# Performance work log

Hardware: AMD Instinct MI355X
Metric: run time of the kernel (lower is better)

The kernel has to match this reference:

```python
import jax, jax.numpy as jnp
import numpy as np

BORDER = 8
NMS_THRESH = 0.0
NMS_KSIZE = 5
TOP_K = 512
GAUSS_KSIZE = 15
GAUSS_SIGMA = 0.5
LOSS_LAMBDA = 1.0


def filter_border(x, border=BORDER):
    B, C, H, W = x.shape
    mask = jnp.zeros((H, W), x.dtype).at[border:H - border, border:W - border].set(1.0)
    return x * mask


def _bilinear_sample(img, x, y):
    # img: [H,W]; x,y: [H,W] float pixel coords in src frame; zeros outside.
    H, W = img.shape
    x0 = jnp.floor(x)
    y0 = jnp.floor(y)
    wx1 = x - x0
    wy1 = y - y0

    def gather(yy, xx):
        valid = (xx >= 0) & (xx <= W - 1) & (yy >= 0) & (yy <= H - 1)
        xi = jnp.clip(xx, 0, W - 1).astype(jnp.int32)
        yi = jnp.clip(yy, 0, H - 1).astype(jnp.int32)
        return img[yi, xi] * valid.astype(img.dtype)

    return ((1 - wy1) * (1 - wx1) * gather(y0, x0)
            + (1 - wy1) * wx1 * gather(y0, x0 + 1)
            + wy1 * (1 - wx1) * gather(y0 + 1, x0)
            + wy1 * wx1 * gather(y0 + 1, x0 + 1))


def warp_image(ref, src, homo):
    # Sample src at homo-mapped coords of ref's pixel grid -> output in ref frame.
    B, _, H, W = ref.shape
    ys, xs = jnp.meshgrid(jnp.arange(H, dtype=ref.dtype), jnp.arange(W, dtype=ref.dtype), indexing='ij')
    pts = jnp.stack([xs.ravel(), ys.ravel(), jnp.ones(H * W, ref.dtype)], 0)  # [3, HW]
    mapped = jnp.einsum('bij,jn->bin', homo, pts)  # [B,3,HW]
    x = (mapped[:, 0] / mapped[:, 2]).reshape(B, H, W)
    y = (mapped[:, 1] / mapped[:, 2]).reshape(B, H, W)
    out = jax.vmap(_bilinear_sample)(src[:, 0], x, y)  # [B,H,W]
    return out[:, None]


def select_keypoints(score, thresh, ksize, top_k):
    B, _, H, W = score.shape
    pooled = jax.lax.reduce_window(score, -jnp.inf, jax.lax.max,
                                   (1, 1, ksize, ksize), (1, 1, 1, 1), 'SAME')
    keep = (score == pooled) & (score > thresh)
    s = jnp.where(keep, score, 0.0)
    flat = s.reshape(B, H * W)
    vals, idx = jax.lax.top_k(flat, top_k)
    out = jnp.zeros_like(flat).at[jnp.arange(B)[:, None], idx].set(vals)
    kp = jnp.stack([idx // W, idx % W], -1)  # [B, top_k, 2] (y, x)
    return out.reshape(B, 1, H, W), kp


def gaussian_filter(x, ksize, sigma):
    ax = jnp.arange(ksize, dtype=x.dtype) - (ksize - 1) / 2.0
    g = jnp.exp(-(ax ** 2) / (2.0 * sigma ** 2))
    g = g / g.sum()
    k2 = jnp.outer(g, g)[None, None]  # [1,1,k,k]
    return jax.lax.conv_general_dilated(x, k2, (1, 1), 'SAME')


def setup_inputs() -> dict:
    key = jax.random.key(0)
    k1, k2, k3 = jax.random.split(key, 3)
    B, H, W = 16, 480, 640
    score1 = jax.random.uniform(k1, (B, 1, H, W), jnp.float32)
    score2 = jax.random.uniform(k2, (B, 1, H, W), jnp.float32)
    # Near-identity pixel-space homographies: small rotation/shear/perspective + a few px translation.
    scale = jnp.array([[0.01, 0.01, 2.0],
                       [0.01, 0.01, 2.0],
                       [1e-5, 1e-5, 0.0]], jnp.float32)
    homo12 = jnp.eye(3, dtype=jnp.float32) + jax.random.normal(k3, (B, 3, 3), jnp.float32) * scale
    return {"score1": score1, "score2": score2, "homo12": homo12}


def reference(score1, score2, homo12):
    score2 = filter_border(score2)
    w_score2 = warp_image(score1, score2, homo12)
    vis_mask = jnp.ones_like(score2)
    vis_mask1 = (warp_image(score1, vis_mask, homo12) > 0).astype(score1.dtype)
    s1, kp1 = select_keypoints(score1, NMS_THRESH, NMS_KSIZE, TOP_K)
    s1 = gaussian_filter(s1, GAUSS_KSIZE, GAUSS_SIGMA)
    gt_s1, _ = select_keypoints(w_score2, NMS_THRESH, NMS_KSIZE, TOP_K)
    gt_s1 = gaussian_filter(gt_s1, GAUSS_KSIZE, GAUSS_SIGMA)
    norm = vis_mask1.sum()
    loss = (((s1 - gt_s1) ** 2) * vis_mask1 / norm).sum() * LOSS_LAMBDA
    return (loss, kp1, vis_mask1)
```

## Files before the change

### kernel.cpp

```cpp
#include <hip/hip_runtime.h>
#include <cstdint>
#include <cstddef>

#define BN 16
#define HH 480
#define WW 640
#define HWSZ (HH*WW)
#define CAP 32768
#define TOPK 512
#define RED_BLOCKS 2048
#define NTX 64
#define NTY 32

typedef unsigned long long u64;

#define W2_OFF   0ULL
#define W2_SZ    ((unsigned long long)BN*HWSZ*4ULL)
#define MAPS_OFF (W2_OFF + W2_SZ)
#define MAPS_SZ  (2ULL*BN*HWSZ*4ULL)
#define CAND_OFF (MAPS_OFF + MAPS_SZ)
#define CAND_SZ  (2ULL*BN*CAP*8ULL)
#define CNT_OFF  (CAND_OFF + CAND_SZ)
#define CNT_SZ   (4096ULL)
#define SEL_OFF  (CNT_OFF + CNT_SZ)
#define SEL_SZ   (2ULL*BN*TOPK*8ULL)
#define PART_OFF (SEL_OFF + SEL_SZ)
#define PART_SZ  ((unsigned long long)RED_BLOCKS*2*4ULL)

__global__ void k_warp_vis(const float* __restrict__ score2,
                           const float* __restrict__ homo,
                           float* __restrict__ w2,
                           float* __restrict__ vis,
                           unsigned int* __restrict__ cnt,
                           float* __restrict__ maps) {
    if (blockIdx.x == 0) {
        for (int i = threadIdx.x; i < 1024; i += 256) cnt[i] = 0u;
    }
    int t = blockIdx.x * 256 + threadIdx.x;
    {
        float4 z4 = make_float4(0.f, 0.f, 0.f, 0.f);
        *reinterpret_cast<float4*>(maps + (size_t)t * 8)     = z4;
        *reinterpret_cast<float4*>(maps + (size_t)t * 8 + 4) = z4;
    }
    int b = t / (HWSZ / 4);
    int q = t - b * (HWSZ / 4);
    int p = q * 4;
    int py = p / WW, px = p - py * WW;
    const float* h = homo + b * 9;
    const float* sb = score2 + (size_t)b * HWSZ;

    float4 wout;
    float vout[4];
    #pragma unroll
    for (int u = 0; u < 4; ++u) {
        float fx = (float)(px + u), fy = (float)py;
        float X = h[0] * fx + h[1] * fy + h[2];
        float Y = h[3] * fx + h[4] * fy + h[5];
        float Z = h[6] * fx + h[7] * fy + h[8];
        float x = X / Z, y = Y / Z;
        float x0 = floorf(x), y0 = floorf(y);
        float wx = x - x0, wy = y - y0;
        float vv[4], gv[4];
        #pragma unroll
        for (int j = 0; j < 2; ++j) {
            #pragma unroll
            for (int i = 0; i < 2; ++i) {
                float xx = x0 + (float)i;
                float yy = y0 + (float)j;
                bool valid = (xx >= 0.f) && (xx <= (float)(WW - 1)) &&
                             (yy >= 0.f) && (yy <= (float)(HH - 1));
                int xi = (int)fminf(fmaxf(xx, 0.f), (float)(WW - 1));
                int yi = (int)fminf(fmaxf(yy, 0.f), (float)(HH - 1));
                float v = sb[yi * WW + xi];
                bool inb = (xi >= 8) && (xi < WW - 8) && (yi >= 8) && (yi < HH - 8);
                vv[j * 2 + i] = (valid && inb) ? v : 0.f;
                gv[j * 2 + i] = valid ? 1.f : 0.f;
            }
        }
        float w00 = (1.f - wy) * (1.f - wx), w01 = (1.f - wy) * wx;
        float w10 = wy * (1.f - wx),         w11 = wy * wx;
        float val = w00 * vv[0] + w01 * vv[1] + w10 * vv[2] + w11 * vv[3];
        float vsm = w00 * gv[0] + w01 * gv[1] + w10 * gv[2] + w11 * gv[3];
        ((float*)&wout)[u] = val;
        vout[u] = (vsm > 0.f) ? 1.f : 0.f;
    }
    int base = b * HWSZ + p;
    *reinterpret_cast<float4*>(w2 + base) = wout;
    vis[base + 0] = vout[0];
    vis[base + 1] = vout[1];
    vis[base + 2] = vout[2];
    vis[base + 3] = vout[3];
}

__global__ void k_nms(const float* __restrict__ s1,
                      const float* __restrict__ w2,
                      u64* __restrict__ cand,
                      unsigned int* __restrict__ cnt) {
    __shared__ float tile[NTY + 4][NTX + 4];
    __shared__ float colmax[NTY][NTX + 4];
    __shared__ unsigned int s_loc, s_base;
    int z = blockIdx.z;
    const float* sb = (z < BN) ? (s1 + (size_t)z * HWSZ)
                               : (w2 + (size_t)(z - BN) * HWSZ);
    int tid = threadIdx.x;
    int bx0 = blockIdx.x * NTX, by0 = blockIdx.y * NTY;
    if (tid == 0) s_loc = 0;

    for (int i = tid; i < (NTY + 4) * (NTX + 4); i += 256) {
        int ly = i / (NTX + 4), lx = i - ly * (NTX + 4);
        int gy = by0 + ly - 2, gx = bx0 + lx - 2;
        float v = -__builtin_inff();
        if ((unsigned)gy < (unsigned)HH && (unsigned)gx < (unsigned)WW)
            v = sb[gy * WW + gx];
        tile[ly][lx] = v;
    }
    __syncthreads();

    for (int i = tid; i < NTY * (NTX + 4); i += 256) {
        int y = i / (NTX + 4), x = i - y * (NTX + 4);
        float m = tile[y][x];
        m = fmaxf(m, tile[y + 1][x]);
        m = fmaxf(m, tile[y + 2][x]);
        m = fmaxf(m, tile[y + 3][x]);
        m = fmaxf(m, tile[y + 4][x]);
        colmax[y][x] = m;
    }
    __syncthreads();

    int ox = tid & 63, oyb = (tid >> 6) * 8;
    bool fl[8];
    float vv[8];
    unsigned int pos[8];
    #pragma unroll
    for (int k = 0; k < 8; ++k) {
        int oy = oyb + k;
        float v = tile[oy + 2][ox + 2];
        float m = colmax[oy][ox];
        m = fmaxf(m, colmax[oy][ox + 1]);
        m = fmaxf(m, colmax[oy][ox + 2]);
        m = fmaxf(m, colmax[oy][ox + 3]);
        m = fmaxf(m, colmax[oy][ox + 4]);
        fl[k] = (v == m) && (v > 0.f);
        vv[k] = v;
        if (fl[k]) pos[k] = atomicAdd(&s_loc, 1u);
    }
    __syncthreads();
    if (tid == 0 && s_loc) s_base = atomicAdd(&cnt[z * 32], s_loc);
    __syncthreads();
    #pragma unroll
    for (int k = 0; k < 8; ++k) {
        if (fl[k]) {
            unsigned int off = s_base + pos[k];
            if (off < CAP) {
                int p = (by0 + oyb + k) * WW + bx0 + ox;
                cand[(size_t)z * CAP + off] =
                    ((u64)__float_as_uint(vv[k]) << 32) | (u64)(~(unsigned)p);
            }
        }
    }
}

__global__ __launch_bounds__(1024) void k_topk(const u64* __restrict__ cand,
                                               const unsigned int* __restrict__ cnt,
                                               u64* __restrict__ sel,
                                               float* __restrict__ kp_out) {
    int s = blockIdx.x;
    int tid = threadIdx.x;
    int n = (int)cnt[s * 32];
    if (n > CAP) n = CAP;
    const u64* keys = cand + (size_t)s * CAP;

    __shared__ unsigned int histw[16][256];
    __shared__ unsigned int hist[256];
    __shared__ u64 skeys[TOPK];
    __shared__ int s_digit, s_krem, s_done;
    __shared__ unsigned int s_cnt;

    int wid = tid >> 6;

    if (n > TOPK) {
        u64 prefix = 0ULL;
        int krem = TOPK;
        for (int lvl = 7; lvl >= 0; --lvl) {
            for (int i = tid; i < 16 * 256; i += 1024) ((unsigned int*)histw)[i] = 0u;
            if (tid == 0) s_done = 0;
            __syncthreads();
            int shift = lvl * 8;
            u64 pmask = (lvl == 7) ? 0ULL : (~0ULL << (shift + 8));
            for (int i = tid; i < n; i += 1024) {
                u64 k = keys[i];
                if ((k & pmask) == prefix)
                    atomicAdd(&histw[wid][(unsigned int)((k >> shift) & 0xFF)], 1u);
            }
            __syncthreads();
            if (tid < 256) {
                unsigned int sum = 0;
                #pragma unroll
                for (int w = 0; w < 16; ++w) sum += histw[w][tid];
                hist[tid] = sum;
            }
            __syncthreads();
            for (int off = 1; off < 256; off <<= 1) {
                unsigned int add = 0;
                if (tid < 256 - off) add = hist[tid + off];
                __syncthreads();
                if (tid < 256) hist[tid] += add;
                __syncthreads();
            }
            if (tid < 256) {
                unsigned int ge = hist[tid];
                unsigned int gt = (tid < 255) ? hist[tid + 1] : 0u;
                if (ge >= (unsigned)krem && gt < (unsigned)krem) {
                    s_digit = tid; s_krem = krem - (int)gt;
                    if (ge == (unsigned)krem) s_done = 1;
                }
            }
            __syncthreads();
            prefix |= ((u64)s_digit) << shift;
            krem = s_krem;
            int done = s_done;
            __syncthreads();
            if (done) break;
        }
        if (tid == 0) s_cnt = 0;
        __syncthreads();
        for (int i = tid; i < n; i += 1024) {
            u64 k = keys[i];
            if (k >= prefix) {
                unsigned int pos = atomicAdd(&s_cnt, 1u);
                if (pos < TOPK) skeys[pos] = k;
            }
        }
        __syncthreads();
        for (int i = (int)s_cnt + tid; i < TOPK; i += 1024) skeys[i] = 0ULL;
    } else {
        for (int i = tid; i < TOPK; i += 1024) skeys[i] = (i < n) ? keys[i] : 0ULL;
    }
    __syncthreads();

    if (s < BN) {
        for (int k = 2; k <= TOPK; k <<= 1) {
            for (int j = k >> 1; j > 0; j >>= 1) {
                if (tid < 256) {
                    int i = (tid % j) + (tid / j) * (j << 1);
                    int l = i + j;
                    bool desc = ((i & k) == 0);
                    u64 a = skeys[i], c = skeys[l];
                    if ((a < c) == desc) { skeys[i] = c; skeys[l] = a; }
                }
                __syncthreads();
            }
        }
    }

    for (int i = tid; i < TOPK; i += 1024) {
        u64 k = skeys[i];
        sel[(size_t)s * TOPK + i] = k;
        if (s < BN) {
            unsigned int idx = ~(unsigned int)(k & 0xFFFFFFFFULL);
            int y = (int)(idx / WW), x = (int)(idx - (unsigned int)y * WW);
            kp_out[(size_t)(s * TOPK + i) * 2 + 0] = (float)y;
            kp_out[(size_t)(s * TOPK + i) * 2 + 1] = (float)x;
        }
    }
}

__global__ void k_stamp(const u64* __restrict__ sel,
                        float* __restrict__ maps) {
    int idx = blockIdx.x * 256 + threadIdx.x;
    int gi = idx / 225;
    int t  = idx - gi * 225;
    u64 k = sel[gi];
    float val = __uint_as_float((unsigned int)(k >> 32));
    if (val <= 0.f) return;
    unsigned int pidx = ~(unsigned int)(k & 0xFFFFFFFFULL);
    int py = (int)(pidx / WW), px = (int)(pidx - (unsigned int)py * WW);
    int dy = t / 15 - 7, dx = t - (dy + 7) * 15 - 7;
    int yy = py + dy, xx = px + dx;
    if (yy < 0 || yy >= HH || xx < 0 || xx >= WW) return;
    const float inv_s2 = 0.61869347f;
    float ga = __expf(-2.f * (float)(dy * dy));
    float gb = __expf(-2.f * (float)(dx * dx));
    int m = gi >> 13, b = (gi >> 9) & 15;
    atomicAdd(&maps[((size_t)m * BN + b) * HWSZ + yy * WW + xx], val * ga * gb * inv_s2);
}

__global__ void k_reduce(const float* __restrict__ maps,
                         const float* __restrict__ vis,
                         float* __restrict__ partial) {
    const int N = BN * HWSZ;
    float lp = 0.f, vsum = 0.f;
    int stride = RED_BLOCKS * 256 * 4;
    for (int i = (blockIdx.x * 256 + threadIdx.x) * 4; i < N; i += stride) {
        float4 m0 = *reinterpret_cast<const float4*>(maps + i);
        float4 m1 = *reinterpret_cast<const float4*>(maps + N + i);
        float v0 = vis[i + 0], v1 = vis[i + 1], v2 = vis[i + 2], v3 = vis[i + 3];
        float d0 = m0.x - m1.x, d1 = m0.y - m1.y, d2 = m0.z - m1.z, d3 = m0.w - m1.w;
        lp += d0 * d0 * v0 + d1 * d1 * v1 + d2 * d2 * v2 + d3 * d3 * v3;
        vsum += v0 + v1 + v2 + v3;
    }
    #pragma unroll
    for (int off = 32; off > 0; off >>= 1) {
        lp   += __shfl_down(lp, off);
        vsum += __shfl_down(vsum, off);
    }
    __shared__ float sl[4], sv[4];
    int w = threadIdx.x >> 6, ln = threadIdx.x & 63;
    if (ln == 0) { sl[w] = lp; sv[w] = vsum; }
    __syncthreads();
    if (threadIdx.x == 0) {
        partial[blockIdx.x * 2 + 0] = sl[0] + sl[1] + sl[2] + sl[3];
        partial[blockIdx.x * 2 + 1] = sv[0] + sv[1] + sv[2] + sv[3];
    }
}

__global__ void k_final(const float* __restrict__ partial, float* __restrict__ out) {
    float a = 0.f, c = 0.f;
    for (int i = threadIdx.x; i < RED_BLOCKS; i += 256) {
        a += partial[i * 2 + 0];
        c += partial[i * 2 + 1];
    }
    #pragma unroll
    for (int off = 32; off > 0; off >>= 1) {
        a += __shfl_down(a, off);
        c += __shfl_down(c, off);
    }
    __shared__ float sl[4], sv[4];
    int w = threadIdx.x >> 6, ln = threadIdx.x & 63;
    if (ln == 0) { sl[w] = a; sv[w] = c; }
    __syncthreads();
    if (threadIdx.x == 0)
        out[0] = (sl[0] + sl[1] + sl[2] + sl[3]) / (sv[0] + sv[1] + sv[2] + sv[3]);
}

extern "C" void kernel_launch(void* const* d_in, const int* in_sizes, int n_in,
                              void* d_out, int out_size, void* d_ws, size_t ws_size,
                              hipStream_t stream) {
    const float* score1 = (const float*)d_in[0];
    const float* score2 = (const float*)d_in[1];
    const float* homo   = (const float*)d_in[2];
    float* out = (float*)d_out;
    char* ws = (char*)d_ws;

    float* w2          = (float*)(ws + W2_OFF);
    float* maps        = (float*)(ws + MAPS_OFF);
    u64* cand          = (u64*)(ws + CAND_OFF);
    unsigned int* cnt  = (unsigned int*)(ws + CNT_OFF);
    u64* sel           = (u64*)(ws + SEL_OFF);
    float* partial     = (float*)(ws + PART_OFF);

    float* kp_out  = out + 1;
    float* vis_out = out + 1 + (size_t)BN * TOPK * 2;

    k_warp_vis<<<BN * HWSZ / (256 * 4), 256, 0, stream>>>(score2, homo, w2, vis_out, cnt, maps);

    dim3 g(WW / NTX, HH / NTY, 2 * BN);
    k_nms<<<g, 256, 0, stream>>>(score1, w2, cand, cnt);

    k_topk<<<32, 1024, 0, stream>>>(cand, cnt, sel, kp_out);

    k_stamp<<<(2 * BN * TOPK * 225) / 256, 256, 0, stream>>>(sel, maps);

    k_reduce<<<RED_BLOCKS, 256, 0, stream>>>(maps, vis_out, partial);
    k_final<<<1, 256, 0, stream>>>(partial, out);
}
```

Measured before the change: 202.7 us.

## Compact top-k candidates into shared memory, ballot NMS offsets, fuse final reduction

Top-k radix select now copies the surviving candidates into a shared-memory buffer once the selected bucket is small enough, so later histogram passes read shared memory instead of rescanning global memory. The scan over 256 bins uses a single-wave shuffle scan in place of a barrier-heavy shared-memory loop. NMS uses wave ballots and popcounts instead of per-element shared atomics. The final loss reduction is folded into the last k_reduce block via an atomic counter, which removes one launch but relies on that counter being zeroed each call.

```diff
diff --git a/kernel.cpp b/kernel.cpp
--- a/kernel.cpp
+++ b/kernel.cpp
@@ -11,6 +11,7 @@
 #define RED_BLOCKS 2048
 #define NTX 64
 #define NTY 32
+#define CBUF 1536
 
 typedef unsigned long long u64;
 
@@ -98,13 +99,13 @@
                       unsigned int* __restrict__ cnt) {
     __shared__ float tile[NTY + 4][NTX + 4];
     __shared__ float colmax[NTY][NTX + 4];
-    __shared__ unsigned int s_loc, s_base;
+    __shared__ unsigned int wcnt[4];
+    __shared__ unsigned int s_base;
     int z = blockIdx.z;
     const float* sb = (z < BN) ? (s1 + (size_t)z * HWSZ)
                                : (w2 + (size_t)(z - BN) * HWSZ);
     int tid = threadIdx.x;
     int bx0 = blockIdx.x * NTX, by0 = blockIdx.y * NTY;
-    if (tid == 0) s_loc = 0;
 
     for (int i = tid; i < (NTY + 4) * (NTX + 4); i += 256) {
         int ly = i / (NTX + 4), lx = i - ly * (NTX + 4);
@@ -128,9 +129,12 @@
     __syncthreads();
 
     int ox = tid & 63, oyb = (tid >> 6) * 8;
+    int wid = tid >> 6, lane = tid & 63;
+    u64 lt_mask = (1ULL << lane) - 1ULL;
     bool fl[8];
     float vv[8];
-    unsigned int pos[8];
+    unsigned int off_k[8];
+    unsigned int wtot = 0;
     #pragma unroll
     for (int k = 0; k < 8; ++k) {
         int oy = oyb + k;
@@ -142,15 +146,24 @@
         m = fmaxf(m, colmax[oy][ox + 4]);
         fl[k] = (v == m) && (v > 0.f);
         vv[k] = v;
-        if (fl[k]) pos[k] = atomicAdd(&s_loc, 1u);
-    }
-    __syncthreads();
-    if (tid == 0 && s_loc) s_base = atomicAdd(&cnt[z * 32], s_loc);
+        u64 bal = __ballot(fl[k]);
+        off_k[k] = wtot + (unsigned)__popcll(bal & lt_mask);
+        wtot += (unsigned)__popcll(bal);
+    }
+    if (lane == 0) wcnt[wid] = wtot;
+    __syncthreads();
+    if (tid == 0) {
+        unsigned tot = wcnt[0] + wcnt[1] + wcnt[2] + wcnt[3];
+        unsigned base = tot ? atomicAdd(&cnt[z * 32], tot) : 0u;
+        unsigned acc = base;
+        #pragma unroll
+        for (int w = 0; w < 4; ++w) { unsigned c = wcnt[w]; wcnt[w] = acc; acc += c; }
+    }
     __syncthreads();
     #pragma unroll
     for (int k = 0; k < 8; ++k) {
         if (fl[k]) {
-            unsigned int off = s_base + pos[k];
+            unsigned off = wcnt[wid] + off_k[k];
             if (off < CAP) {
                 int p = (by0 + oyb + k) * WW + bx0 + ox;
                 cand[(size_t)z * CAP + off] =
@@ -168,27 +181,31 @@
     int tid = threadIdx.x;
     int n = (int)cnt[s * 32];
     if (n > CAP) n = CAP;
-    const u64* keys = cand + (size_t)s * CAP;
+    const u64* gkeys = cand + (size_t)s * CAP;
 
     __shared__ unsigned int histw[16][256];
     __shared__ unsigned int hist[256];
     __shared__ u64 skeys[TOPK];
-    __shared__ int s_digit, s_krem, s_done;
+    __shared__ u64 cbuf[CBUF];
+    __shared__ int s_digit, s_krem, s_done, s_ge, s_nc;
     __shared__ unsigned int s_cnt;
 
-    int wid = tid >> 6;
+    int wid = tid >> 6, lane = tid & 63;
 
     if (n > TOPK) {
         u64 prefix = 0ULL;
         int krem = TOPK;
+        bool comp = false;
+        int nsrc = n;
         for (int lvl = 7; lvl >= 0; --lvl) {
             for (int i = tid; i < 16 * 256; i += 1024) ((unsigned int*)histw)[i] = 0u;
             if (tid == 0) s_done = 0;
             __syncthreads();
+            const u64* src = comp ? cbuf : gkeys;
             int shift = lvl * 8;
             u64 pmask = (lvl == 7) ? 0ULL : (~0ULL << (shift + 8));
-            for (int i = tid; i < n; i += 1024) {
-                u64 k = keys[i];
+            for (int i = tid; i < nsrc; i += 1024) {
+                u64 k = src[i];
                 if ((k & pmask) == prefix)
                     atomicAdd(&histw[wid][(unsigned int)((k >> shift) & 0xFF)], 1u);
             }
@@ -200,32 +217,58 @@
                 hist[tid] = sum;
             }
             __syncthreads();
-            for (int off = 1; off < 256; off <<= 1) {
-                unsigned int add = 0;
-                if (tid < 256 - off) add = hist[tid + off];
-                __syncthreads();
-                if (tid < 256) hist[tid] += add;
-                __syncthreads();
-            }
-            if (tid < 256) {
-                unsigned int ge = hist[tid];
-                unsigned int gt = (tid < 255) ? hist[tid + 1] : 0u;
-                if (ge >= (unsigned)krem && gt < (unsigned)krem) {
-                    s_digit = tid; s_krem = krem - (int)gt;
-                    if (ge == (unsigned)krem) s_done = 1;
+            if (tid < 64) {
+                unsigned c0 = hist[4 * lane + 0], c1 = hist[4 * lane + 1];
+                unsigned c2 = hist[4 * lane + 2], c3 = hist[4 * lane + 3];
+                unsigned s3 = c3, s2 = c2 + s3, s1 = c1 + s2, s0 = c0 + s1;
+                unsigned g = s0;
+                #pragma unroll
+                for (int off = 1; off < 64; off <<= 1) {
+                    unsigned t2 = __shfl(g, (lane + off) & 63);
+                    g += (lane + off < 64) ? t2 : 0u;
                 }
+                unsigned above = g - s0;
+                unsigned ge[4] = { s0 + above, s1 + above, s2 + above, s3 + above };
+                unsigned gt[4] = { s1 + above, s2 + above, s3 + above, above };
+                unsigned kr = (unsigned)krem;
+                #pragma unroll
+                for (int j = 0; j < 4; ++j) {
+                    if (ge[j] >= kr && gt[j] < kr) {
+                        s_digit = 4 * lane + j;
+                        s_krem = (int)(kr - gt[j]);
+                        s_ge = (int)ge[j];
+                        if (ge[j] == kr) s_done = 1;
+                    }
+                }
             }
             __syncthreads();
+            int krem_old = krem;
             prefix |= ((u64)s_digit) << shift;
             krem = s_krem;
             int done = s_done;
+            int ge_sel = s_ge;
             __syncthreads();
             if (done) break;
+            if (!comp && (TOPK - krem_old) + ge_sel <= CBUF) {
+                if (tid == 0) s_nc = 0;
+                __syncthreads();
+                for (int i = tid; i < nsrc; i += 1024) {
+                    u64 k = gkeys[i];
+                    if (k >= prefix) {
+                        unsigned pos = atomicAdd((unsigned int*)&s_nc, 1u);
+                        if ((int)pos < CBUF) cbuf[pos] = k;
+                    }
+                }
+                __syncthreads();
+                comp = true;
+                nsrc = s_nc;
+            }
         }
         if (tid == 0) s_cnt = 0;
         __syncthreads();
-        for (int i = tid; i < n; i += 1024) {
-            u64 k = keys[i];
+        const u64* fsrc = comp ? cbuf : gkeys;
+        for (int i = tid; i < nsrc; i += 1024) {
+            u64 k = fsrc[i];
             if (k >= prefix) {
                 unsigned int pos = atomicAdd(&s_cnt, 1u);
                 if (pos < TOPK) skeys[pos] = k;
@@ -234,7 +277,7 @@
         __syncthreads();
         for (int i = (int)s_cnt + tid; i < TOPK; i += 1024) skeys[i] = 0ULL;
     } else {
-        for (int i = tid; i < TOPK; i += 1024) skeys[i] = (i < n) ? keys[i] : 0ULL;
+        for (int i = tid; i < TOPK; i += 1024) skeys[i] = (i < n) ? gkeys[i] : 0ULL;
     }
     __syncthreads();
 
@@ -287,7 +330,9 @@
 
 __global__ void k_reduce(const float* __restrict__ maps,
                          const float* __restrict__ vis,
-                         float* __restrict__ partial) {
+                         float* __restrict__ partial,
+                         unsigned int* __restrict__ done_ctr,
+                         float* __restrict__ out) {
     const int N = BN * HWSZ;
     float lp = 0.f, vsum = 0.f;
     int stride = RED_BLOCKS * 256 * 4;
@@ -305,32 +350,34 @@
         vsum += __shfl_down(vsum, off);
     }
     __shared__ float sl[4], sv[4];
+    __shared__ unsigned int s_last;
     int w = threadIdx.x >> 6, ln = threadIdx.x & 63;
     if (ln == 0) { sl[w] = lp; sv[w] = vsum; }
     __syncthreads();
     if (threadIdx.x == 0) {
         partial[blockIdx.x * 2 + 0] = sl[0] + sl[1] + sl[2] + sl[3];
         partial[blockIdx.x * 2 + 1] = sv[0] + sv[1] + sv[2] + sv[3];
-    }
-}
-
-__global__ void k_final(const float* __restrict__ partial, float* __restrict__ out) {
-    float a = 0.f, c = 0.f;
-    for (int i = threadIdx.x; i < RED_BLOCKS; i += 256) {
-        a += partial[i * 2 + 0];
-        c += partial[i * 2 + 1];
-    }
-    #pragma unroll
-    for (int off = 32; off > 0; off >>= 1) {
-        a += __shfl_down(a, off);
-        c += __shfl_down(c, off);
-    }
-    __shared__ float sl[4], sv[4];
-    int w = threadIdx.x >> 6, ln = threadIdx.x & 63;
-    if (ln == 0) { sl[w] = a; sv[w] = c; }
-    __syncthreads();
-    if (threadIdx.x == 0)
-        out[0] = (sl[0] + sl[1] + sl[2] + sl[3]) / (sv[0] + sv[1] + sv[2] + sv[3]);
+        __threadfence();
+        s_last = atomicAdd(done_ctr, 1u);
+    }
+    __syncthreads();
+    if (s_last == RED_BLOCKS - 1) {
+        __threadfence();
+        float a = 0.f, c = 0.f;
+        for (int i = threadIdx.x; i < RED_BLOCKS; i += 256) {
+            a += partial[i * 2 + 0];
+            c += partial[i * 2 + 1];
+        }
+        #pragma unroll
+        for (int off = 32; off > 0; off >>= 1) {
+            a += __shfl_down(a, off);
+            c += __shfl_down(c, off);
+        }
+        if (ln == 0) { sl[w] = a; sv[w] = c; }
+        __syncthreads();
+        if (threadIdx.x == 0)
+            out[0] = (sl[0] + sl[1] + sl[2] + sl[3]) / (sv[0] + sv[1] + sv[2] + sv[3]);
+    }
 }
 
 extern "C" void kernel_launch(void* const* d_in, const int* in_sizes, int n_in,
@@ -361,6 +408,5 @@
 
     k_stamp<<<(2 * BN * TOPK * 225) / 256, 256, 0, stream>>>(sel, maps);
 
-    k_reduce<<<RED_BLOCKS, 256, 0, stream>>>(maps, vis_out, partial);
-    k_final<<<1, 256, 0, stream>>>(partial, out);
-}
+    k_reduce<<<RED_BLOCKS, 256, 0, stream>>>(maps, vis_out, partial, &cnt[1023], out);
+}
```

Result: slower. 250.4 us (+23.5%).
